# Kernel tuning notes

Hardware: AMD Instinct MI355X
Metric: run time of the kernel (lower is better)

The kernel has to match this reference:

```python
import jax, jax.numpy as jnp
import numpy as np

INPUT_SIZE = 1024
HEAD_SIZE = 64


def setup_inputs() -> dict:
    key = jax.random.key(0)
    kx, kk, kq, kv = jax.random.split(key, 4)
    B, T, C, H = 4, 4096, INPUT_SIZE, HEAD_SIZE
    x = jax.random.normal(kx, (B, T, C), dtype=jnp.float32)
    # nn.Linear(C, H, bias=False) weight is (H, C); we store transposed (C, H)
    # so that y = x @ W matches torch's x @ weight.T
    scale = 1.0 / np.sqrt(C)
    Wk = jax.random.uniform(kk, (C, H), dtype=jnp.float32, minval=-scale, maxval=scale)
    Wq = jax.random.uniform(kq, (C, H), dtype=jnp.float32, minval=-scale, maxval=scale)
    Wv = jax.random.uniform(kv, (C, H), dtype=jnp.float32, minval=-scale, maxval=scale)
    return {"x": x, "Wk": Wk, "Wq": Wq, "Wv": Wv}


def reference(x, Wk, Wq, Wv):
    B, T, C = x.shape
    k = x @ Wk  # (B, T, H)
    q = x @ Wq
    v = x @ Wv
    H = k.shape[-1]
    # scaled scores (B, T, T)
    wei = jnp.einsum('bth,bsh->bts', q, k) * (H ** -0.5)
    causal = jnp.tril(jnp.ones((T, T), dtype=bool))
    wei = jnp.where(causal, wei, -jnp.inf)
    wei = jax.nn.softmax(wei, axis=-1)
    out = jnp.einsum('bts,bsh->bth', wei, v)  # (B, T, H)
    return out
```

## Files before the change

kernel.cpp:

```cpp
#include <hip/hip_runtime.h>
#include <math.h>


#define BT   16384
#define TDIM 4096
#define CDIM 1024
#define HDIM 64
#define ACCW 68

typedef __attribute__((ext_vector_type(8))) short bf16x8;
typedef __attribute__((ext_vector_type(4))) float f32x4;
typedef __attribute__((ext_vector_type(8))) unsigned short us8;
typedef __attribute__((ext_vector_type(4))) unsigned short us4;

static __device__ __forceinline__ unsigned short f2bf(float f) {
    unsigned int u = __float_as_uint(f);
    u += 0x7fffu + ((u >> 16) & 1u);
    return (unsigned short)(u >> 16);
}

__global__ __launch_bounds__(256) void wtrans_zero(
    const float* __restrict__ Wk, const float* __restrict__ Wq,
    const float* __restrict__ Wv, unsigned short* __restrict__ wtg,
    float* __restrict__ accp)
{
    int idx = blockIdx.x * 256 + threadIdx.x;
    int mat = idx >> 16;
    int rem = idx & 65535;
    int h = rem >> 10, c = rem & 1023;
    const float* W = (mat == 0) ? Wk : (mat == 1) ? Wq : Wv;
    wtg[idx] = f2bf(W[c * HDIM + h]);
    for (int i = idx; i < BT * ACCW; i += 196608) accp[i] = 0.f;
}

__global__ __launch_bounds__(512) void qkv_proj(
    const float* __restrict__ x, const unsigned short* __restrict__ wtg,
    unsigned short* __restrict__ kg, unsigned short* __restrict__ qg,
    unsigned short* __restrict__ vtg)
{
    __shared__ __align__(16) unsigned short xs[32][72];
    __shared__ __align__(16) unsigned short wts[192][72];
    const int t = threadIdx.x;
    const int lane = t & 63, wv = t >> 6, quad = lane >> 4, l16 = lane & 15;
    const int mt = wv >> 2;
    const int nq = wv & 3;
    const int row0 = blockIdx.x * 32;

    const int xr = t >> 4, xc4 = (t & 15) * 4;
    const int wn = t >> 3, wc8 = (t & 7) * 8;

    f32x4 acc3[3];
    #pragma unroll
    for (int i = 0; i < 3; i++) acc3[i] = (f32x4){0.f, 0.f, 0.f, 0.f};

    float4 xv = *(const float4*)&x[(size_t)(row0 + xr) * CDIM + xc4];
    us8 w0 = *(const us8*)&wtg[(size_t)(wn +   0) * CDIM + wc8];
    us8 w1 = *(const us8*)&wtg[(size_t)(wn +  64) * CDIM + wc8];
    us8 w2 = *(const us8*)&wtg[(size_t)(wn + 128) * CDIM + wc8];

    for (int cc = 0; cc < CDIM; cc += 64) {
        __syncthreads();
        us4 pk = { f2bf(xv.x), f2bf(xv.y), f2bf(xv.z), f2bf(xv.w) };
        *(us4*)&xs[xr][xc4] = pk;
        *(us8*)&wts[wn +   0][wc8] = w0;
        *(us8*)&wts[wn +  64][wc8] = w1;
        *(us8*)&wts[wn + 128][wc8] = w2;
        __syncthreads();
        if (cc + 64 < CDIM) {
            int nc = cc + 64;
            xv = *(const float4*)&x[(size_t)(row0 + xr) * CDIM + nc + xc4];
            w0 = *(const us8*)&wtg[(size_t)(wn +   0) * CDIM + nc + wc8];
            w1 = *(const us8*)&wtg[(size_t)(wn +  64) * CDIM + nc + wc8];
            w2 = *(const us8*)&wtg[(size_t)(wn + 128) * CDIM + nc + wc8];
        }
        bf16x8 a0 = *(const bf16x8*)&xs[mt * 16 + l16][quad * 8];
        bf16x8 a1 = *(const bf16x8*)&xs[mt * 16 + l16][32 + quad * 8];
        #pragma unroll
        for (int j = 0; j < 3; j++) {
            int nt = nq * 3 + j;
            bf16x8 b0 = *(const bf16x8*)&wts[nt * 16 + l16][quad * 8];
            bf16x8 b1 = *(const bf16x8*)&wts[nt * 16 + l16][32 + quad * 8];
            acc3[j] = __builtin_amdgcn_mfma_f32_16x16x32_bf16(a0, b0, acc3[j], 0, 0, 0);
            acc3[j] = __builtin_amdgcn_mfma_f32_16x16x32_bf16(a1, b1, acc3[j], 0, 0, 0);
        }
    }

    const int mrow = row0 + mt * 16 + quad * 4;
    #pragma unroll
    for (int j = 0; j < 3; j++) {
        int nt = nq * 3 + j;
        int mat = nt >> 2;
        int col = (nt & 3) * 16 + l16;
        #pragma unroll
        for (int reg = 0; reg < 4; reg++) {
            int r = mrow + reg;
            unsigned short bv = f2bf(acc3[j][reg]);
            if (mat == 0)      kg[(size_t)r * HDIM + col] = bv;
            else if (mat == 1) qg[(size_t)r * HDIM + col] = bv;
            else {
                int bb = r >> 12, tr = r & 4095;
                vtg[((size_t)(bb * HDIM + col) << 12) + tr] = bv;
            }
        }
    }
}

__global__ __launch_bounds__(256) void attn(
    const unsigned short* __restrict__ qg, const unsigned short* __restrict__ kg,
    const unsigned short* __restrict__ vtg, float* __restrict__ accp)
{
    __shared__ __align__(16) unsigned short Ks[64][72];
    __shared__ __align__(16) unsigned short Vt[80][72];
    __shared__ __align__(16) unsigned short Ps[4][16][72];

    const int t = threadIdx.x;
    const int lane = t & 63, wv = t >> 6, quad = lane >> 4, l16 = lane & 15;

    const int b = blockIdx.x / 160;
    const int s = blockIdx.x - b * 160;
    int qt, c;
    if (s < 16)      { qt = s;               c = 0; }
    else if (s < 48) { int u = s - 16; qt = 16 + (u >> 1); c = u & 1; }
    else if (s < 96) { int u = s - 48; int q3 = u / 3; qt = 32 + q3; c = u - 3 * q3; }
    else             { int u = s - 96; qt = 48 + (u >> 2); c = u & 3; }

    const size_t bbase = (size_t)b * TDIM;
    const int Q0 = qt * 64;
    const int kt0 = c * 16;
    const int kt1 = (kt0 + 15 < qt) ? kt0 + 15 : qt;

    for (int i = t; i < 16 * 72; i += 256) {
        int r = i / 72, cc = i - r * 72;
        Vt[64 + r][cc] = (r == 0) ? (unsigned short)0x3F80 : (unsigned short)0;
    }

    const int qrow = Q0 + wv * 16 + l16;
    bf16x8 qa0 = *(const bf16x8*)&qg[(bbase + qrow) * HDIM + quad * 8];
    bf16x8 qa1 = *(const bf16x8*)&qg[(bbase + qrow) * HDIM + 32 + quad * 8];

    f32x4 O[5];
    #pragma unroll
    for (int i = 0; i < 5; i++) O[i] = (f32x4){0.f, 0.f, 0.f, 0.f};

    const int fr = t >> 3, fc = (t & 7) * 8;

    us8 kr0 = *(const us8*)&kg[(bbase + kt0 * 64 + fr) * HDIM + fc];
    us8 kr1 = *(const us8*)&kg[(bbase + kt0 * 64 + fr + 32) * HDIM + fc];
    us8 vr0 = *(const us8*)&vtg[((size_t)(b * HDIM + fr) << 12) + kt0 * 64 + fc];
    us8 vr1 = *(const us8*)&vtg[((size_t)(b * HDIM + fr + 32) << 12) + kt0 * 64 + fc];

    const int rbase = wv * 16 + quad * 4;
    for (int kt = kt0; kt <= kt1; kt++) {
        __syncthreads();
        *(us8*)&Ks[fr][fc] = kr0;
        *(us8*)&Ks[fr + 32][fc] = kr1;
        *(us8*)&Vt[fr][fc] = vr0;
        *(us8*)&Vt[fr + 32][fc] = vr1;
        __syncthreads();
        if (kt < kt1) {
            int kn = kt + 1;
            kr0 = *(const us8*)&kg[(bbase + kn * 64 + fr) * HDIM + fc];
            kr1 = *(const us8*)&kg[(bbase + kn * 64 + fr + 32) * HDIM + fc];
            vr0 = *(const us8*)&vtg[((size_t)(b * HDIM + fr) << 12) + kn * 64 + fc];
            vr1 = *(const us8*)&vtg[((size_t)(b * HDIM + fr + 32) << 12) + kn * 64 + fc];
        }

        f32x4 sT[4];
        #pragma unroll
        for (int st = 0; st < 4; st++) {
            bf16x8 kb0 = *(const bf16x8*)&Ks[st * 16 + l16][quad * 8];
            bf16x8 kb1 = *(const bf16x8*)&Ks[st * 16 + l16][32 + quad * 8];
            f32x4 z = (f32x4){0.f, 0.f, 0.f, 0.f};
            z = __builtin_amdgcn_mfma_f32_16x16x32_bf16(qa0, kb0, z, 0, 0, 0);
            z = __builtin_amdgcn_mfma_f32_16x16x32_bf16(qa1, kb1, z, 0, 0, 0);
            sT[st] = z;
        }
        const bool diag = (kt == qt);
        #pragma unroll
        for (int st = 0; st < 4; st++) {
            int col = st * 16 + l16;
            #pragma unroll
            for (int r = 0; r < 4; r++) {
                float p = (diag && (col > rbase + r)) ? 0.f
                                                      : __expf(sT[st][r] * 0.125f);
                Ps[wv][quad * 4 + r][col] = f2bf(p);
            }
        }
        bf16x8 pa0 = *(const bf16x8*)&Ps[wv][l16][quad * 8];
        bf16x8 pa1 = *(const bf16x8*)&Ps[wv][l16][32 + quad * 8];
        #pragma unroll
        for (int nt = 0; nt < 5; nt++) {
            bf16x8 vb0 = *(const bf16x8*)&Vt[nt * 16 + l16][quad * 8];
            bf16x8 vb1 = *(const bf16x8*)&Vt[nt * 16 + l16][32 + quad * 8];
            O[nt] = __builtin_amdgcn_mfma_f32_16x16x32_bf16(pa0, vb0, O[nt], 0, 0, 0);
            O[nt] = __builtin_amdgcn_mfma_f32_16x16x32_bf16(pa1, vb1, O[nt], 0, 0, 0);
        }
    }

    const int grow = (b << 12) + Q0 + wv * 16 + quad * 4;
    #pragma unroll
    for (int nt = 0; nt < 4; nt++)
        #pragma unroll
        for (int r = 0; r < 4; r++)
            atomicAdd(&accp[(size_t)(grow + r) * ACCW + nt * 16 + l16], O[nt][r]);
    if (l16 == 0) {
        #pragma unroll
        for (int r = 0; r < 4; r++)
            atomicAdd(&accp[(size_t)(grow + r) * ACCW + 64], O[4][r]);
    }
}

__global__ __launch_bounds__(256) void normalize(
    const float* __restrict__ accp, float* __restrict__ out)
{
    int idx = blockIdx.x * 256 + threadIdx.x;
    int row = idx >> 4, c4 = (idx & 15) * 4;
    float inv = 1.f / accp[(size_t)row * ACCW + 64];
    float4 o = *(const float4*)&accp[(size_t)row * ACCW + c4];
    float4 res = make_float4(o.x * inv, o.y * inv, o.z * inv, o.w * inv);
    *(float4*)&out[(size_t)row * HDIM + c4] = res;
}

extern "C" void kernel_launch(void* const* d_in, const int* in_sizes, int n_in,
                              void* d_out, int out_size, void* d_ws, size_t ws_size,
                              hipStream_t stream) {
    const float* x  = (const float*)d_in[0];
    const float* Wk = (const float*)d_in[1];
    const float* Wq = (const float*)d_in[2];
    const float* Wv = (const float*)d_in[3];
    float* out = (float*)d_out;

    unsigned short* wtg = (unsigned short*)d_ws;
    unsigned short* kg  = wtg + 196608;
    unsigned short* qg  = kg + (size_t)BT * HDIM;
    unsigned short* vtg = qg + (size_t)BT * HDIM;
    float* accp = (float*)(vtg + (size_t)4 * HDIM * TDIM);

    wtrans_zero<<<768, 256, 0, stream>>>(Wk, Wq, Wv, wtg, accp);
    qkv_proj<<<BT / 32, 512, 0, stream>>>(x, wtg, kg, qg, vtg);
    attn<<<4 * 160, 256, 0, stream>>>(qg, kg, vtg, accp);
    normalize<<<BT * HDIM / (4 * 256), 256, 0, stream>>>(accp, out);
}
```

Before: 151.5 us.

## Keep softmax P in registers via transposed score MFMA and permlane swaps

Computes the score tile transposed (K as the A operand) so each lane holds scores for one query row. The probabilities are packed to bf16 with v_cvt_pk_bf16_f32 and rearranged into the PV MFMA operand layout with permlane32/16 swaps, removing the per-wave shared-memory round trip for P. The 1/sqrt(H) scale is folded into Q during projection, and V-transpose stores are vectorised to 4-wide. The risk is that the lane permutation must exactly match the MFMA operand layout, which is hardware-specific.

```diff
diff --git a/kernel.cpp b/kernel.cpp
--- a/kernel.cpp
+++ b/kernel.cpp
@@ -17,6 +17,11 @@
     unsigned int u = __float_as_uint(f);
     u += 0x7fffu + ((u >> 16) & 1u);
     return (unsigned short)(u >> 16);
+}
+
+static __device__ __forceinline__ void pswap(unsigned &x, unsigned &y) {
+    asm("v_permlane32_swap_b32 %0, %1" : "+v"(x), "+v"(y));
+    asm("v_permlane16_swap_b32 %0, %1" : "+v"(x), "+v"(y));
 }
 
 __global__ __launch_bounds__(256) void wtrans_zero(
@@ -91,16 +96,17 @@
         int nt = nq * 3 + j;
         int mat = nt >> 2;
         int col = (nt & 3) * 16 + l16;
-        #pragma unroll
-        for (int reg = 0; reg < 4; reg++) {
-            int r = mrow + reg;
-            unsigned short bv = f2bf(acc3[j][reg]);
-            if (mat == 0)      kg[(size_t)r * HDIM + col] = bv;
-            else if (mat == 1) qg[(size_t)r * HDIM + col] = bv;
-            else {
-                int bb = r >> 12, tr = r & 4095;
-                vtg[((size_t)(bb * HDIM + col) << 12) + tr] = bv;
-            }
+        if (mat == 2) {
+            int bb = mrow >> 12, tr = mrow & 4095;
+            us4 pv = { f2bf(acc3[j][0]), f2bf(acc3[j][1]),
+                       f2bf(acc3[j][2]), f2bf(acc3[j][3]) };
+            *(us4*)&vtg[((size_t)(bb * HDIM + col) << 12) + tr] = pv;
+        } else {
+            float s = (mat == 1) ? 0.125f : 1.0f;
+            unsigned short* dst = (mat == 0) ? kg : qg;
+            #pragma unroll
+            for (int reg = 0; reg < 4; reg++)
+                dst[(size_t)(mrow + reg) * HDIM + col] = f2bf(acc3[j][reg] * s);
         }
     }
 }
@@ -111,7 +117,6 @@
 {
     __shared__ __align__(16) unsigned short Ks[64][72];
     __shared__ __align__(16) unsigned short Vt[80][72];
-    __shared__ __align__(16) unsigned short Ps[4][16][72];
 
     const int t = threadIdx.x;
     const int lane = t & 63, wv = t >> 6, quad = lane >> 4, l16 = lane & 15;
@@ -149,7 +154,7 @@
     us8 vr0 = *(const us8*)&vtg[((size_t)(b * HDIM + fr) << 12) + kt0 * 64 + fc];
     us8 vr1 = *(const us8*)&vtg[((size_t)(b * HDIM + fr + 32) << 12) + kt0 * 64 + fc];
 
-    const int rbase = wv * 16 + quad * 4;
+    const int qloc = wv * 16 + l16;
     for (int kt = kt0; kt <= kt1; kt++) {
         __syncthreads();
         *(us8*)&Ks[fr][fc] = kr0;
@@ -171,23 +176,41 @@
             bf16x8 kb0 = *(const bf16x8*)&Ks[st * 16 + l16][quad * 8];
             bf16x8 kb1 = *(const bf16x8*)&Ks[st * 16 + l16][32 + quad * 8];
             f32x4 z = (f32x4){0.f, 0.f, 0.f, 0.f};
-            z = __builtin_amdgcn_mfma_f32_16x16x32_bf16(qa0, kb0, z, 0, 0, 0);
-            z = __builtin_amdgcn_mfma_f32_16x16x32_bf16(qa1, kb1, z, 0, 0, 0);
+            z = __builtin_amdgcn_mfma_f32_16x16x32_bf16(kb0, qa0, z, 0, 0, 0);
+            z = __builtin_amdgcn_mfma_f32_16x16x32_bf16(kb1, qa1, z, 0, 0, 0);
             sT[st] = z;
         }
+
         const bool diag = (kt == qt);
+        float p[4][4];
         #pragma unroll
         for (int st = 0; st < 4; st++) {
-            int col = st * 16 + l16;
             #pragma unroll
             for (int r = 0; r < 4; r++) {
-                float p = (diag && (col > rbase + r)) ? 0.f
-                                                      : __expf(sT[st][r] * 0.125f);
-                Ps[wv][quad * 4 + r][col] = f2bf(p);
+                int kkloc = st * 16 + quad * 4 + r;
+                p[st][r] = (diag && (kkloc > qloc)) ? 0.f : __expf(sT[st][r]);
             }
         }
-        bf16x8 pa0 = *(const bf16x8*)&Ps[wv][l16][quad * 8];
-        bf16x8 pa1 = *(const bf16x8*)&Ps[wv][l16][32 + quad * 8];
+
+        unsigned cpk[4][2];
+        #pragma unroll
+        for (int st = 0; st < 4; st++) {
+            asm("v_cvt_pk_bf16_f32 %0, %1, %2"
+                : "=v"(cpk[st][0]) : "v"(p[st][0]), "v"(p[st][1]));
+            asm("v_cvt_pk_bf16_f32 %0, %1, %2"
+                : "=v"(cpk[st][1]) : "v"(p[st][2]), "v"(p[st][3]));
+        }
+        union { unsigned u[4]; bf16x8 v; } pa0u, pa1u;
+        {
+            unsigned a0 = cpk[0][0], b0 = cpk[1][0]; pswap(a0, b0);
+            unsigned a1 = cpk[0][1], b1 = cpk[1][1]; pswap(a1, b1);
+            pa0u.u[0] = a0; pa0u.u[1] = a1; pa0u.u[2] = b0; pa0u.u[3] = b1;
+            unsigned a2 = cpk[2][0], b2 = cpk[3][0]; pswap(a2, b2);
+            unsigned a3 = cpk[2][1], b3 = cpk[3][1]; pswap(a3, b3);
+            pa1u.u[0] = a2; pa1u.u[1] = a3; pa1u.u[2] = b2; pa1u.u[3] = b3;
+        }
+        const bf16x8 pa0 = pa0u.v, pa1 = pa1u.v;
+
         #pragma unroll
         for (int nt = 0; nt < 5; nt++) {
             bf16x8 vb0 = *(const bf16x8*)&Vt[nt * 16 + l16][quad * 8];
```

New measurement: 144.1 us. 4.9% less time.
